# Kernel tuning notes

Measured on AMD Instinct MI355X. Metric: run time of the kernel, lower is better.

The kernel has to match this reference:

```python
import jax, jax.numpy as jnp
import numpy as np

N, D, T, P, NP, H = 200000, 128, 8, 2000, 9, 2048


def setup_inputs() -> dict:
    key = jax.random.key(0)
    ks = jax.random.split(key, 12)
    inp = {
        'motion_z': jax.random.normal(ks[0], (N, D), jnp.float32),
        'tasks': jax.random.randint(ks[1], (N,), 0, T, jnp.int32),
        'tasks_mask': jax.random.randint(ks[2], (N,), 0, 2, jnp.int32),
        'patient_ids': jax.random.randint(ks[3], (N,), 0, P, jnp.int32),
        'phenos': jax.random.uniform(ks[4], (N, NP), jnp.float32),
        'phenos_mask': jax.random.randint(ks[5], (N,), 0, 2, jnp.int32),
        'W1': jax.random.normal(ks[6], (T * D, H), jnp.float32) * 0.02,
        'b1': jnp.zeros((H,), jnp.float32),
        'W2': jax.random.normal(ks[7], (H, H), jnp.float32) * 0.02,
        'b2': jnp.zeros((H,), jnp.float32),
        'W3': jax.random.normal(ks[8], (H, NP), jnp.float32) * 0.02,
        'b3': jnp.zeros((NP,), jnp.float32),
    }
    return inp


def _fingerprint(motion_z, tasks, tasks_mask, patient_ids, phenos, phenos_mask):
    # valid sample mask (tasks_mask==1 & patient id present & phenos_mask==1)
    valid = (tasks_mask == 1) & (phenos_mask == 1)
    w = valid.astype(motion_z.dtype)                      # [N]
    wz = motion_z * w[:, None]                            # [N, D]

    # global per-task mean (fallback for empty patient-task cells)
    t_sum = jax.ops.segment_sum(wz, tasks, num_segments=T)           # [T, D]
    t_cnt = jax.ops.segment_sum(w, tasks, num_segments=T)            # [T]
    task_mean = t_sum / jnp.maximum(t_cnt, 1.0)[:, None]             # [T, D]

    # fused (patient, task) segment mean — single pass scatter-reduce
    seg = patient_ids * T + tasks                                    # [N]
    pt_sum = jax.ops.segment_sum(wz, seg, num_segments=P * T)        # [P*T, D]
    pt_cnt = jax.ops.segment_sum(w, seg, num_segments=P * T)         # [P*T]
    pt_mean = pt_sum / jnp.maximum(pt_cnt, 1.0)[:, None]
    pt_mean = jnp.where((pt_cnt > 0)[:, None], pt_mean,
                        jnp.tile(task_mean, (P, 1)))                 # fallback
    fingerprint = pt_mean.reshape(P, T * D)

    # first valid pheno row per patient (phenos_id_each[0])
    idxs = jnp.where(valid, jnp.arange(N), N)
    first = jnp.full((P,), N, jnp.int32).at[patient_ids].min(idxs.astype(jnp.int32))
    uni_phenos = phenos[jnp.clip(first, 0, N - 1)]                   # [P, NP]
    return fingerprint, uni_phenos


def reference(motion_z, tasks, tasks_mask, patient_ids, phenos, phenos_mask,
              W1, b1, W2, b2, W3, b3):
    fingerprint, uni_phenos = _fingerprint(
        motion_z, tasks, tasks_mask, patient_ids, phenos, phenos_mask)
    h = jax.nn.relu(fingerprint @ W1 + b1)
    h = jax.nn.relu(h @ W2 + b2)
    pheno_latent = h @ W3 + b3
    out = jax.nn.sigmoid(pheno_latent)
    return out, uni_phenos, pheno_latent
```

## Files before the change

kernel.cpp:

```cpp
#include <hip/hip_runtime.h>
#include <math.h>

#define N_SAMP 200000
#define D_     128
#define T_     8
#define P_     2000
#define NP_    9
#define H_     2048
#define MPAD   2048
#define NSEG   16000
#define NSEGP  16384

#define OFF_CNT     0
#define OFF_CURSOR  65536
#define OFF_OFFS    131072
#define OFF_FIRST   196608
#define OFF_PERM    204800
#define OFF_TMEAN   1004800
#define OFF_TSUM    1008896
#define OFF_TCNT    1012992
#define OFF_PTSUM   1013760
#define OFF_FPHI    9205760
#define OFF_FPLO    13400064
#define OFF_W1THI   17594368
#define OFF_W1TLO   21788672
#define OFF_H1HI    25982976
#define OFF_H1LO    34371584
#define OFF_W2THI   42760192
#define OFF_W2TLO   51148800
#define OFF_H2      OFF_FPHI

typedef __attribute__((ext_vector_type(8))) short bf16x8;
typedef __attribute__((ext_vector_type(4))) float f32x4;

__device__ __forceinline__ unsigned f2bf_rne(float x) {
    unsigned b = __float_as_uint(x);
    return (b + 0x7fffu + ((b >> 16) & 1u)) >> 16;
}
__device__ __forceinline__ float bf2f(unsigned u) {
    return __uint_as_float(u << 16);
}

__device__ __forceinline__ void gload16(const void* g, void* l) {
    __builtin_amdgcn_global_load_lds(
        (const __attribute__((address_space(1))) unsigned int*)g,
        (__attribute__((address_space(3))) unsigned int*)l, 16, 0, 0);
}

__global__ __launch_bounds__(256) void hist_first(
    const int* __restrict__ tasks, const int* __restrict__ tmask,
    const int* __restrict__ pids, const int* __restrict__ pmask,
    int* __restrict__ cnt, int* __restrict__ first)
{
    int i = blockIdx.x * 256 + threadIdx.x;
    if (i >= N_SAMP) return;
    if (tmask[i] != 1 || pmask[i] != 1) return;
    int p = pids[i];
    atomicAdd(&cnt[p * T_ + tasks[i]], 1);
    atomicMin(&first[p], i);
}

__global__ __launch_bounds__(256) void scan16k(
    const int* __restrict__ cnt, int* __restrict__ offs)
{
    __shared__ int part[256];
    int tid = threadIdx.x;
    int base = tid * 64;
    int s = 0;
#pragma unroll 8
    for (int j = 0; j < 64; ++j) s += cnt[base + j];
    part[tid] = s;
    __syncthreads();
    for (int d = 1; d < 256; d <<= 1) {
        int v = (tid >= d) ? part[tid - d] : 0;
        __syncthreads();
        part[tid] += v;
        __syncthreads();
    }
    int run = (tid > 0) ? part[tid - 1] : 0;
    for (int j = 0; j < 64; ++j) {
        offs[base + j] = run;
        run += cnt[base + j];
    }
}

__global__ __launch_bounds__(256) void scatter_idx(
    const int* __restrict__ tasks, const int* __restrict__ tmask,
    const int* __restrict__ pids, const int* __restrict__ pmask,
    const int* __restrict__ offs, int* __restrict__ cursor,
    int* __restrict__ perm)
{
    int i = blockIdx.x * 256 + threadIdx.x;
    if (i >= N_SAMP) return;
    if (tmask[i] != 1 || pmask[i] != 1) return;
    int seg = pids[i] * T_ + tasks[i];
    int pos = atomicAdd(&cursor[seg], 1);
    perm[offs[seg] + pos] = i;
}

__global__ __launch_bounds__(256) void gather_cell(
    const float* __restrict__ motion_z, const int* __restrict__ cnt,
    const int* __restrict__ offs, const int* __restrict__ perm,
    float* __restrict__ pt_sum)
{
    int wid  = (blockIdx.x * 256 + threadIdx.x) >> 6;
    int lane = threadIdx.x & 63;
    if (wid >= NSEG) return;
    int c = cnt[wid], base = offs[wid];
    float2 acc = make_float2(0.f, 0.f);
    for (int r = 0; r < c; ++r) {
        int idx = perm[base + r];
        float2 v = *(const float2*)&motion_z[(size_t)idx * D_ + lane * 2];
        acc.x += v.x; acc.y += v.y;
    }
    *(float2*)&pt_sum[(size_t)wid * D_ + lane * 2] = acc;
}

__global__ __launch_bounds__(256) void tsum_partial(
    const float* __restrict__ pt_sum, const int* __restrict__ cnt,
    float* __restrict__ tsum, float* __restrict__ tcnt)
{
    int p0 = blockIdx.x * 16;
    int tid = threadIdx.x;
    float4 acc = make_float4(0.f, 0.f, 0.f, 0.f);
    for (int pl = 0; pl < 16; ++pl) {
        float4 v = *(const float4*)&pt_sum[(size_t)(p0 + pl) * 1024 + tid * 4];
        acc.x += v.x; acc.y += v.y; acc.z += v.z; acc.w += v.w;
    }
    atomicAdd(&tsum[tid * 4 + 0], acc.x);
    atomicAdd(&tsum[tid * 4 + 1], acc.y);
    atomicAdd(&tsum[tid * 4 + 2], acc.z);
    atomicAdd(&tsum[tid * 4 + 3], acc.w);
    if (tid < 128) {
        int p = p0 + (tid >> 3), t = tid & 7;
        atomicAdd(&tcnt[t], (float)cnt[p * 8 + t]);
    }
}

__global__ __launch_bounds__(256) void tmean_gather(
    const float* __restrict__ tsum, const float* __restrict__ tcnt,
    float* __restrict__ tmean, const int* __restrict__ first,
    const float* __restrict__ phenos, float* __restrict__ up)
{
    int e = blockIdx.x * 256 + threadIdx.x;
    if (e < 1024) {
        tmean[e] = tsum[e] / fmaxf(tcnt[e >> 7], 1.0f);
    } else {
        int g = e - 1024;
        if (g < P_ * NP_) {
            int p = g / NP_, j = g - p * NP_;
            int idx = first[p];
            if (idx > N_SAMP - 1) idx = N_SAMP - 1;
            up[g] = phenos[(size_t)idx * NP_ + j];
        }
    }
}

__global__ __launch_bounds__(256) void finalize_split(
    const float* __restrict__ pt_sum, const int* __restrict__ cnt,
    const float* __restrict__ tmean,
    unsigned short* __restrict__ fphi, unsigned short* __restrict__ fplo)
{
    int e = blockIdx.x * blockDim.x + threadIdx.x;
    int p = e >> 10, col = e & 1023;
    float v = 0.f;
    if (p < P_) {
        int seg = p * T_ + (col >> 7);
        int c = cnt[seg];
        v = (c > 0) ? pt_sum[e] / (float)c : tmean[col];
    }
    unsigned hi = f2bf_rne(v);
    float lo = v - bf2f(hi);
    fphi[e] = (unsigned short)hi;
    fplo[e] = (unsigned short)f2bf_rne(lo);
}

__global__ __launch_bounds__(256) void conv_w_t(
    const float* __restrict__ W, unsigned short* __restrict__ Whi,
    unsigned short* __restrict__ Wlo, int K, int N)
{
    __shared__ float tile[32][33];
    int k0 = blockIdx.y * 32, n0 = blockIdx.x * 32;
    int r = threadIdx.x >> 3, c4 = (threadIdx.x & 7) * 4;
    float4 v = *(const float4*)&W[(size_t)(k0 + r) * N + n0 + c4];
    tile[r][c4 + 0] = v.x; tile[r][c4 + 1] = v.y;
    tile[r][c4 + 2] = v.z; tile[r][c4 + 3] = v.w;
    __syncthreads();
    unsigned short hi[4], lo[4];
#pragma unroll
    for (int q = 0; q < 4; ++q) {
        float x = tile[c4 + q][r];
        unsigned h = f2bf_rne(x);
        hi[q] = (unsigned short)h;
        lo[q] = (unsigned short)f2bf_rne(x - bf2f(h));
    }
    size_t o = (size_t)(n0 + r) * K + k0 + c4;
    *(ushort4*)&Whi[o] = make_ushort4(hi[0], hi[1], hi[2], hi[3]);
    *(ushort4*)&Wlo[o] = make_ushort4(lo[0], lo[1], lo[2], lo[3]);
}

template<int OUTF32>
__global__ __launch_bounds__(256, 1) void gemm_split(
    const unsigned short* __restrict__ Ahi, const unsigned short* __restrict__ Alo,
    const unsigned short* __restrict__ Bhi, const unsigned short* __restrict__ Blo,
    const float* __restrict__ bias,
    float* __restrict__ Cf, unsigned short* __restrict__ Chi,
    unsigned short* __restrict__ Clo, int K)
{
    __shared__ __align__(16) char lds[2][4][8192];
    int tid  = threadIdx.x;
    int lane = tid & 63, w = tid >> 6;
    int wr = w >> 1, wc = w & 1;
    int row0 = blockIdx.y * 128, col0 = blockIdx.x * 128;

    int fr = lane & 15;
    int fk = (lane >> 4) * 8;

    const unsigned short* srcs[4] = {Ahi, Alo, Bhi, Blo};
    int base0[4] = {row0, row0, col0, col0};

    auto STAGE = [&](int buf, int t) {
        int k0 = t * 32;
#pragma unroll
        for (int pc = 0; pc < 4; ++pc) {
#pragma unroll
            for (int rep = 0; rep < 2; ++rep) {
                int tile = rep * 4 + w;
                const unsigned short* g =
                    srcs[pc] + (size_t)(base0[pc] + tile * 16 + fr) * K + k0 + fk;
                gload16(g, &lds[buf][pc][tile * 1024]);
            }
        }
    };

    f32x4 acc[4][4] = {};
    int nt = K / 32;
    STAGE(0, 0);
    __syncthreads();
    int cur = 0;
    int lo16 = lane * 16;

    for (int t = 0; t < nt; ++t) {
        if (t + 1 < nt) STAGE(cur ^ 1, t + 1);
        bf16x8 ah[4], al[4], bh[4], bl[4];
#pragma unroll
        for (int i = 0; i < 4; ++i) {
            ah[i] = *(const bf16x8*)&lds[cur][0][(wr * 4 + i) * 1024 + lo16];
            al[i] = *(const bf16x8*)&lds[cur][1][(wr * 4 + i) * 1024 + lo16];
        }
#pragma unroll
        for (int j = 0; j < 4; ++j) {
            bh[j] = *(const bf16x8*)&lds[cur][2][(wc * 4 + j) * 1024 + lo16];
            bl[j] = *(const bf16x8*)&lds[cur][3][(wc * 4 + j) * 1024 + lo16];
        }
#pragma unroll
        for (int i = 0; i < 4; ++i)
#pragma unroll
            for (int j = 0; j < 4; ++j) {
                acc[i][j] = __builtin_amdgcn_mfma_f32_16x16x32_bf16(ah[i], bh[j], acc[i][j], 0, 0, 0);
                acc[i][j] = __builtin_amdgcn_mfma_f32_16x16x32_bf16(ah[i], bl[j], acc[i][j], 0, 0, 0);
                acc[i][j] = __builtin_amdgcn_mfma_f32_16x16x32_bf16(al[i], bh[j], acc[i][j], 0, 0, 0);
            }
        __syncthreads();
        cur ^= 1;
    }

#pragma unroll
    for (int i = 0; i < 4; ++i) {
        int r = row0 + wr * 64 + i * 16 + (lane >> 4) * 4;
#pragma unroll
        for (int j = 0; j < 4; ++j) {
            int c = col0 + wc * 64 + j * 16 + (lane & 15);
            float bv = bias[c];
#pragma unroll
            for (int q = 0; q < 4; ++q) {
                float x = fmaxf(acc[i][j][q] + bv, 0.f);
                size_t o = (size_t)(r + q) * H_ + c;
                if (OUTF32) {
                    Cf[o] = x;
                } else {
                    unsigned hb = f2bf_rne(x);
                    Chi[o] = (unsigned short)hb;
                    Clo[o] = (unsigned short)f2bf_rne(x - bf2f(hb));
                }
            }
        }
    }
}

__global__ __launch_bounds__(256) void out_head(
    const float* __restrict__ h2, const float* __restrict__ W3,
    const float* __restrict__ b3, float* __restrict__ out,
    float* __restrict__ latent)
{
    __shared__ float w3s[H_ * NP_];
    int tid = threadIdx.x;
    for (int e = tid * 4; e < H_ * NP_; e += 1024)
        *(float4*)&w3s[e] = *(const float4*)&W3[e];
    __syncthreads();

    int wid  = blockIdx.x * 4 + (tid >> 6);
    int lane = tid & 63;
    if (wid >= P_) return;
    const float* hrow = h2 + (size_t)wid * H_;
    float acc[NP_] = {};
    for (int k = lane; k < H_; k += 64) {
        float h = hrow[k];
#pragma unroll
        for (int j = 0; j < NP_; ++j) acc[j] = fmaf(h, w3s[k * NP_ + j], acc[j]);
    }
#pragma unroll
    for (int off = 32; off > 0; off >>= 1)
#pragma unroll
        for (int j = 0; j < NP_; ++j) acc[j] += __shfl_down(acc[j], off);
    if (lane == 0) {
#pragma unroll
        for (int j = 0; j < NP_; ++j) {
            float v = acc[j] + b3[j];
            latent[wid * NP_ + j] = v;
            out[wid * NP_ + j]    = 1.f / (1.f + expf(-v));
        }
    }
}

extern "C" void kernel_launch(void* const* d_in, const int* in_sizes, int n_in,
                              void* d_out, int out_size, void* d_ws, size_t ws_size,
                              hipStream_t stream)
{
    const float* motion_z = (const float*)d_in[0];
    const int*   tasks    = (const int*)d_in[1];
    const int*   tmask    = (const int*)d_in[2];
    const int*   pids     = (const int*)d_in[3];
    const float* phenos   = (const float*)d_in[4];
    const int*   pmask    = (const int*)d_in[5];
    const float* W1 = (const float*)d_in[6];
    const float* b1 = (const float*)d_in[7];
    const float* W2 = (const float*)d_in[8];
    const float* b2 = (const float*)d_in[9];
    const float* W3 = (const float*)d_in[10];
    const float* b3 = (const float*)d_in[11];

    char* ws = (char*)d_ws;
    int*            cnt    = (int*)  (ws + OFF_CNT);
    int*            cursor = (int*)  (ws + OFF_CURSOR);
    int*            offs   = (int*)  (ws + OFF_OFFS);
    int*            first  = (int*)  (ws + OFF_FIRST);
    int*            perm   = (int*)  (ws + OFF_PERM);
    float*          tmean  = (float*)(ws + OFF_TMEAN);
    float*          tsum   = (float*)(ws + OFF_TSUM);
    float*          tcnt   = (float*)(ws + OFF_TCNT);
    float*          pt_sum = (float*)(ws + OFF_PTSUM);
    unsigned short* fphi   = (unsigned short*)(ws + OFF_FPHI);
    unsigned short* fplo   = (unsigned short*)(ws + OFF_FPLO);
    unsigned short* w1thi  = (unsigned short*)(ws + OFF_W1THI);
    unsigned short* w1tlo  = (unsigned short*)(ws + OFF_W1TLO);
    unsigned short* h1hi   = (unsigned short*)(ws + OFF_H1HI);
    unsigned short* h1lo   = (unsigned short*)(ws + OFF_H1LO);
    unsigned short* w2thi  = (unsigned short*)(ws + OFF_W2THI);
    unsigned short* w2tlo  = (unsigned short*)(ws + OFF_W2TLO);
    float*          h2     = (float*)(ws + OFF_H2);

    float* out    = (float*)d_out;
    float* uni    = out + P_ * NP_;
    float* latent = out + 2 * P_ * NP_;

    hipMemsetAsync(cnt,   0,    2 * NSEGP * 4, stream);
    hipMemsetAsync(first, 0x7f, P_ * 4, stream);
    hipMemsetAsync(tsum,  0,    4096 + 256, stream);

    int nrb = (N_SAMP + 255) / 256;
    hist_first<<<nrb, 256, 0, stream>>>(tasks, tmask, pids, pmask, cnt, first);
    scan16k<<<1, 256, 0, stream>>>(cnt, offs);
    scatter_idx<<<nrb, 256, 0, stream>>>(tasks, tmask, pids, pmask, offs,
                                         cursor, perm);
    gather_cell<<<(NSEG * 64 + 255) / 256, 256, 0, stream>>>(
        motion_z, cnt, offs, perm, pt_sum);
    tsum_partial<<<125, 256, 0, stream>>>(pt_sum, cnt, tsum, tcnt);
    tmean_gather<<<(1024 + P_ * NP_ + 255) / 256, 256, 0, stream>>>(
        tsum, tcnt, tmean, first, phenos, uni);
    finalize_split<<<(MPAD * 1024) / 256, 256, 0, stream>>>(
        pt_sum, cnt, tmean, fphi, fplo);

    conv_w_t<<<dim3(H_ / 32, 1024 / 32), 256, 0, stream>>>(W1, w1thi, w1tlo, 1024, H_);
    conv_w_t<<<dim3(H_ / 32, H_ / 32),   256, 0, stream>>>(W2, w2thi, w2tlo, H_, H_);

    gemm_split<0><<<dim3(H_ / 128, MPAD / 128), 256, 0, stream>>>(
        fphi, fplo, w1thi, w1tlo, b1, nullptr, h1hi, h1lo, 1024);
    gemm_split<1><<<dim3(H_ / 128, MPAD / 128), 256, 0, stream>>>(
        h1hi, h1lo, w2thi, w2tlo, b2, h2, nullptr, nullptr, H_);

    out_head<<<P_ / 4, 256, 0, stream>>>(h2, W3, b3, out, latent);
}
```

Before: 425.0 us.

## Fuse fingerprint pipeline into one cooperative kernel and swizzle GEMM block order

```diff
diff --git a/kernel.cpp b/kernel.cpp
--- a/kernel.cpp
+++ b/kernel.cpp
@@ -1,5 +1,8 @@
 #include <hip/hip_runtime.h>
+#include <hip/hip_cooperative_groups.h>
 #include <math.h>
+
+namespace cg = cooperative_groups;
 
 #define N_SAMP 200000
 #define D_     128
@@ -47,140 +50,134 @@
         (__attribute__((address_space(3))) unsigned int*)l, 16, 0, 0);
 }
 
-__global__ __launch_bounds__(256) void hist_first(
-    const int* __restrict__ tasks, const int* __restrict__ tmask,
-    const int* __restrict__ pids, const int* __restrict__ pmask,
-    int* __restrict__ cnt, int* __restrict__ first)
-{
-    int i = blockIdx.x * 256 + threadIdx.x;
-    if (i >= N_SAMP) return;
-    if (tmask[i] != 1 || pmask[i] != 1) return;
-    int p = pids[i];
-    atomicAdd(&cnt[p * T_ + tasks[i]], 1);
-    atomicMin(&first[p], i);
-}
-
-__global__ __launch_bounds__(256) void scan16k(
-    const int* __restrict__ cnt, int* __restrict__ offs)
-{
+__global__ __launch_bounds__(256) void fingerprint_coop(
+    const float* __restrict__ motion_z, const int* __restrict__ tasks,
+    const int* __restrict__ tmask, const int* __restrict__ pids,
+    const int* __restrict__ pmask, const float* __restrict__ phenos,
+    int* __restrict__ cnt, int* __restrict__ cursor, int* __restrict__ offs,
+    int* __restrict__ first, int* __restrict__ perm,
+    float* __restrict__ tsum, float* __restrict__ tcnt,
+    float* __restrict__ tmean, float* __restrict__ pt_sum,
+    unsigned short* __restrict__ fphi, unsigned short* __restrict__ fplo,
+    float* __restrict__ uni)
+{
+    cg::grid_group grid = cg::this_grid();
     __shared__ int part[256];
-    int tid = threadIdx.x;
-    int base = tid * 64;
-    int s = 0;
+    int tid  = threadIdx.x;
+    int gtid = blockIdx.x * 256 + tid;
+    int gsz  = gridDim.x * 256;
+
+    for (int i = gtid; i < NSEGP; i += gsz) { cnt[i] = 0; cursor[i] = 0; }
+    for (int i = gtid; i < P_;    i += gsz) first[i] = 0x7fffffff;
+    for (int i = gtid; i < 1024;  i += gsz) tsum[i] = 0.f;
+    for (int i = gtid; i < 8;     i += gsz) tcnt[i] = 0.f;
+    grid.sync();
+
+    for (int i = gtid; i < N_SAMP; i += gsz)
+        if (tmask[i] == 1 && pmask[i] == 1) {
+            int p = pids[i];
+            atomicAdd(&cnt[p * T_ + tasks[i]], 1);
+            atomicMin(&first[p], i);
+        }
+    grid.sync();
+
+    if (blockIdx.x == 0) {
+        int base = tid * 64, s = 0;
 #pragma unroll 8
-    for (int j = 0; j < 64; ++j) s += cnt[base + j];
-    part[tid] = s;
-    __syncthreads();
-    for (int d = 1; d < 256; d <<= 1) {
-        int v = (tid >= d) ? part[tid - d] : 0;
+        for (int j = 0; j < 64; ++j) s += cnt[base + j];
+        part[tid] = s;
         __syncthreads();
-        part[tid] += v;
-        __syncthreads();
-    }
-    int run = (tid > 0) ? part[tid - 1] : 0;
-    for (int j = 0; j < 64; ++j) {
-        offs[base + j] = run;
-        run += cnt[base + j];
-    }
-}
-
-__global__ __launch_bounds__(256) void scatter_idx(
-    const int* __restrict__ tasks, const int* __restrict__ tmask,
-    const int* __restrict__ pids, const int* __restrict__ pmask,
-    const int* __restrict__ offs, int* __restrict__ cursor,
-    int* __restrict__ perm)
-{
-    int i = blockIdx.x * 256 + threadIdx.x;
-    if (i >= N_SAMP) return;
-    if (tmask[i] != 1 || pmask[i] != 1) return;
-    int seg = pids[i] * T_ + tasks[i];
-    int pos = atomicAdd(&cursor[seg], 1);
-    perm[offs[seg] + pos] = i;
-}
-
-__global__ __launch_bounds__(256) void gather_cell(
-    const float* __restrict__ motion_z, const int* __restrict__ cnt,
-    const int* __restrict__ offs, const int* __restrict__ perm,
-    float* __restrict__ pt_sum)
-{
-    int wid  = (blockIdx.x * 256 + threadIdx.x) >> 6;
-    int lane = threadIdx.x & 63;
-    if (wid >= NSEG) return;
-    int c = cnt[wid], base = offs[wid];
-    float2 acc = make_float2(0.f, 0.f);
-    for (int r = 0; r < c; ++r) {
-        int idx = perm[base + r];
-        float2 v = *(const float2*)&motion_z[(size_t)idx * D_ + lane * 2];
-        acc.x += v.x; acc.y += v.y;
-    }
-    *(float2*)&pt_sum[(size_t)wid * D_ + lane * 2] = acc;
-}
-
-__global__ __launch_bounds__(256) void tsum_partial(
-    const float* __restrict__ pt_sum, const int* __restrict__ cnt,
-    float* __restrict__ tsum, float* __restrict__ tcnt)
-{
-    int p0 = blockIdx.x * 16;
-    int tid = threadIdx.x;
-    float4 acc = make_float4(0.f, 0.f, 0.f, 0.f);
-    for (int pl = 0; pl < 16; ++pl) {
-        float4 v = *(const float4*)&pt_sum[(size_t)(p0 + pl) * 1024 + tid * 4];
-        acc.x += v.x; acc.y += v.y; acc.z += v.z; acc.w += v.w;
-    }
-    atomicAdd(&tsum[tid * 4 + 0], acc.x);
-    atomicAdd(&tsum[tid * 4 + 1], acc.y);
-    atomicAdd(&tsum[tid * 4 + 2], acc.z);
-    atomicAdd(&tsum[tid * 4 + 3], acc.w);
-    if (tid < 128) {
-        int p = p0 + (tid >> 3), t = tid & 7;
-        atomicAdd(&tcnt[t], (float)cnt[p * 8 + t]);
-    }
-}
-
-__global__ __launch_bounds__(256) void tmean_gather(
-    const float* __restrict__ tsum, const float* __restrict__ tcnt,
-    float* __restrict__ tmean, const int* __restrict__ first,
-    const float* __restrict__ phenos, float* __restrict__ up)
-{
-    int e = blockIdx.x * 256 + threadIdx.x;
-    if (e < 1024) {
-        tmean[e] = tsum[e] / fmaxf(tcnt[e >> 7], 1.0f);
-    } else {
-        int g = e - 1024;
-        if (g < P_ * NP_) {
+        for (int d = 1; d < 256; d <<= 1) {
+            int v = (tid >= d) ? part[tid - d] : 0;
+            __syncthreads();
+            part[tid] += v;
+            __syncthreads();
+        }
+        int run = (tid > 0) ? part[tid - 1] : 0;
+        for (int j = 0; j < 64; ++j) { offs[base + j] = run; run += cnt[base + j]; }
+    }
+    grid.sync();
+
+    for (int i = gtid; i < N_SAMP; i += gsz)
+        if (tmask[i] == 1 && pmask[i] == 1) {
+            int seg = pids[i] * T_ + tasks[i];
+            int pos = atomicAdd(&cursor[seg], 1);
+            perm[offs[seg] + pos] = i;
+        }
+    grid.sync();
+
+    {
+        int wid0 = gtid >> 6, lane = tid & 63, nw = gsz >> 6;
+        for (int c = wid0; c < NSEG; c += nw) {
+            int n = cnt[c], base = offs[c];
+            float2 acc = make_float2(0.f, 0.f);
+            for (int r = 0; r < n; ++r) {
+                int idx = perm[base + r];
+                float2 v = *(const float2*)&motion_z[(size_t)idx * D_ + lane * 2];
+                acc.x += v.x; acc.y += v.y;
+            }
+            *(float2*)&pt_sum[(size_t)c * D_ + lane * 2] = acc;
+        }
+    }
+    grid.sync();
+
+    for (int chunk = blockIdx.x; chunk < 125; chunk += gridDim.x) {
+        int p0 = chunk * 16;
+        float4 acc = make_float4(0.f, 0.f, 0.f, 0.f);
+        for (int pl = 0; pl < 16; ++pl) {
+            float4 v = *(const float4*)&pt_sum[(size_t)(p0 + pl) * 1024 + tid * 4];
+            acc.x += v.x; acc.y += v.y; acc.z += v.z; acc.w += v.w;
+        }
+        atomicAdd(&tsum[tid * 4 + 0], acc.x);
+        atomicAdd(&tsum[tid * 4 + 1], acc.y);
+        atomicAdd(&tsum[tid * 4 + 2], acc.z);
+        atomicAdd(&tsum[tid * 4 + 3], acc.w);
+        if (tid < 128) {
+            int p = p0 + (tid >> 3), t = tid & 7;
+            atomicAdd(&tcnt[t], (float)cnt[p * 8 + t]);
+        }
+    }
+    grid.sync();
+
+    for (int e = gtid; e < 1024 + P_ * NP_; e += gsz) {
+        if (e < 1024) {
+            tmean[e] = tsum[e] / fmaxf(tcnt[e >> 7], 1.0f);
+        } else {
+            int g = e - 1024;
             int p = g / NP_, j = g - p * NP_;
             int idx = first[p];
             if (idx > N_SAMP - 1) idx = N_SAMP - 1;
-            up[g] = phenos[(size_t)idx * NP_ + j];
-        }
-    }
-}
-
-__global__ __launch_bounds__(256) void finalize_split(
-    const float* __restrict__ pt_sum, const int* __restrict__ cnt,
-    const float* __restrict__ tmean,
-    unsigned short* __restrict__ fphi, unsigned short* __restrict__ fplo)
-{
-    int e = blockIdx.x * blockDim.x + threadIdx.x;
-    int p = e >> 10, col = e & 1023;
-    float v = 0.f;
-    if (p < P_) {
-        int seg = p * T_ + (col >> 7);
-        int c = cnt[seg];
-        v = (c > 0) ? pt_sum[e] / (float)c : tmean[col];
-    }
-    unsigned hi = f2bf_rne(v);
-    float lo = v - bf2f(hi);
-    fphi[e] = (unsigned short)hi;
-    fplo[e] = (unsigned short)f2bf_rne(lo);
-}
-
-__global__ __launch_bounds__(256) void conv_w_t(
-    const float* __restrict__ W, unsigned short* __restrict__ Whi,
-    unsigned short* __restrict__ Wlo, int K, int N)
+            uni[g] = phenos[(size_t)idx * NP_ + j];
+        }
+    }
+    grid.sync();
+
+    for (int e = gtid; e < MPAD * 1024; e += gsz) {
+        int p = e >> 10, col = e & 1023;
+        float v = 0.f;
+        if (p < P_) {
+            int c = cnt[p * T_ + (col >> 7)];
+            v = (c > 0) ? pt_sum[e] / (float)c : tmean[col];
+        }
+        unsigned hi = f2bf_rne(v);
+        fphi[e] = (unsigned short)hi;
+        fplo[e] = (unsigned short)f2bf_rne(v - bf2f(hi));
+    }
+}
+
+__global__ __launch_bounds__(256) void conv_w_both(
+    const float* __restrict__ W1, const float* __restrict__ W2,
+    unsigned short* __restrict__ w1hi, unsigned short* __restrict__ w1lo,
+    unsigned short* __restrict__ w2hi, unsigned short* __restrict__ w2lo)
 {
     __shared__ float tile[32][33];
-    int k0 = blockIdx.y * 32, n0 = blockIdx.x * 32;
+    int id = blockIdx.x;
+    const float* W; unsigned short *Whi, *Wlo; int K;
+    if (id < 2048) { W = W1; Whi = w1hi; Wlo = w1lo; K = 1024; }
+    else { id -= 2048; W = W2; Whi = w2hi; Wlo = w2lo; K = 2048; }
+    int bx = id & 63, by = id >> 6;
+    int k0 = by * 32, n0 = bx * 32;
+    const int N = 2048;
     int r = threadIdx.x >> 3, c4 = (threadIdx.x & 7) * 4;
     float4 v = *(const float4*)&W[(size_t)(k0 + r) * N + n0 + c4];
     tile[r][c4 + 0] = v.x; tile[r][c4 + 1] = v.y;
@@ -211,7 +208,9 @@
     int tid  = threadIdx.x;
     int lane = tid & 63, w = tid >> 6;
     int wr = w >> 1, wc = w & 1;
-    int row0 = blockIdx.y * 128, col0 = blockIdx.x * 128;
+    int wg = blockIdx.x;
+    int sw = ((wg & 7) << 5) + (wg >> 3);
+    int row0 = (sw >> 4) * 128, col0 = (sw & 15) * 128;
 
     int fr = lane & 15;
     int fk = (lane >> 4) * 8;
@@ -364,29 +363,20 @@
     float* uni    = out + P_ * NP_;
     float* latent = out + 2 * P_ * NP_;
 
-    hipMemsetAsync(cnt,   0,    2 * NSEGP * 4, stream);
-    hipMemsetAsync(first, 0x7f, P_ * 4, stream);
-    hipMemsetAsync(tsum,  0,    4096 + 256, stream);
-
-    int nrb = (N_SAMP + 255) / 256;
-    hist_first<<<nrb, 256, 0, stream>>>(tasks, tmask, pids, pmask, cnt, first);
-    scan16k<<<1, 256, 0, stream>>>(cnt, offs);
-    scatter_idx<<<nrb, 256, 0, stream>>>(tasks, tmask, pids, pmask, offs,
-                                         cursor, perm);
-    gather_cell<<<(NSEG * 64 + 255) / 256, 256, 0, stream>>>(
-        motion_z, cnt, offs, perm, pt_sum);
-    tsum_partial<<<125, 256, 0, stream>>>(pt_sum, cnt, tsum, tcnt);
-    tmean_gather<<<(1024 + P_ * NP_ + 255) / 256, 256, 0, stream>>>(
-        tsum, tcnt, tmean, first, phenos, uni);
-    finalize_split<<<(MPAD * 1024) / 256, 256, 0, stream>>>(
-        pt_sum, cnt, tmean, fphi, fplo);
-
-    conv_w_t<<<dim3(H_ / 32, 1024 / 32), 256, 0, stream>>>(W1, w1thi, w1tlo, 1024, H_);
-    conv_w_t<<<dim3(H_ / 32, H_ / 32),   256, 0, stream>>>(W2, w2thi, w2tlo, H_, H_);
-
-    gemm_split<0><<<dim3(H_ / 128, MPAD / 128), 256, 0, stream>>>(
+    void* cargs[] = {
+        (void*)&motion_z, (void*)&tasks, (void*)&tmask, (void*)&pids,
+        (void*)&pmask, (void*)&phenos, (void*)&cnt, (void*)&cursor,
+        (void*)&offs, (void*)&first, (void*)&perm, (void*)&tsum,
+        (void*)&tcnt, (void*)&tmean, (void*)&pt_sum, (void*)&fphi,
+        (void*)&fplo, (void*)&uni};
+    hipLaunchCooperativeKernel((void*)fingerprint_coop, dim3(512), dim3(256),
+                               cargs, 0, stream);
+
+    conv_w_both<<<6144, 256, 0, stream>>>(W1, W2, w1thi, w1tlo, w2thi, w2tlo);
+
+    gemm_split<0><<<256, 256, 0, stream>>>(
         fphi, fplo, w1thi, w1tlo, b1, nullptr, h1hi, h1lo, 1024);
-    gemm_split<1><<<dim3(H_ / 128, MPAD / 128), 256, 0, stream>>>(
+    gemm_split<1><<<256, 256, 0, stream>>>(
         h1hi, h1lo, w2thi, w2tlo, b2, h2, nullptr, nullptr, H_);
 
     out_head<<<P_ / 4, 256, 0, stream>>>(h2, W3, b3, out, latent);
```

Result: slower. 793.7 us (+86.7%).
